# Kernel optimization log

Measured on AMD Instinct MI355X. Metric: run time of the kernel, lower is better.

The kernel has to match this reference:

```python
import jax, jax.numpy as jnp
from jax import lax
import numpy as np

B, POINTS, FEATURES = 8, 32768, 256
F_DIM = FEATURES // 16  # out_dim of query/key 1x1 convs


def setup_inputs() -> dict:
    key = jax.random.key(0)
    ks = jax.random.split(key, 10)
    s = 0.05
    return {
        "x": jax.random.normal(ks[0], (B, POINTS, FEATURES), jnp.float32),
        "Wq": jax.random.normal(ks[1], (F_DIM, FEATURES), jnp.float32) * s,
        "bq": jax.random.normal(ks[2], (F_DIM,), jnp.float32) * s,
        "Wk": jax.random.normal(ks[3], (F_DIM, FEATURES), jnp.float32) * s,
        "bk": jax.random.normal(ks[4], (F_DIM,), jnp.float32) * s,
        "Wv": jax.random.normal(ks[5], (FEATURES, FEATURES), jnp.float32) * s,
        "bv": jax.random.normal(ks[6], (FEATURES,), jnp.float32) * s,
        "Wup": jax.random.normal(ks[7], (1, 1, 3, 3), jnp.float32) * s,  # torch (in,out,kh,kw)
        "bup": jax.random.normal(ks[8], (1,), jnp.float32) * s,
        "gamma": jax.random.normal(ks[9], (), jnp.float32) * 0.1,  # torch inits to 0; nonzero for testing
    }


def _conv_transpose_s16(x, w, b):
    # torch ConvTranspose2d(1,1,kernel=3,stride=16,padding=0,output_padding=13)
    # == dilated conv with lhs_dilation=16, pad (k-1-p, k-1-p+op) = (2,15), flipped kernel
    k = jnp.flip(w, axis=(2, 3)).transpose(1, 0, 2, 3)  # -> OIHW
    y = lax.conv_general_dilated(
        x, k, window_strides=(1, 1), padding=[(2, 15), (2, 15)],
        lhs_dilation=(16, 16), dimension_numbers=("NCHW", "OIHW", "NCHW"))
    return y + b.reshape(1, -1, 1, 1)


def reference(x, Wq, bq, Wk, bk, Wv, bv, Wup, bup, gamma):
    Bm, points, features = x.shape
    f = features // 16
    # torch: x.view(B, features, -1, 1) -- raw memory reinterpretation, not transpose
    x1 = x.reshape(Bm, features, points)
    # 1x1 convs (dilation irrelevant for kernel_size=1) == channel matmuls
    q = jnp.einsum("of,bfp->bop", Wq, x1) + bq[None, :, None]      # (B, f, points)
    k = jnp.einsum("of,bfp->bop", Wk, x1) + bk[None, :, None]      # (B, f, points)
    k = k.reshape(Bm, points, f)                                    # torch .view reinterpretation
    energy = jnp.einsum("bfp,bpg->bfg", q, k)                       # (B, f, f)
    re_scale = _conv_transpose_s16(energy[:, None], Wup, bup)[:, 0]  # (B, features, features)
    attention = jax.nn.softmax(re_scale, axis=1)
    v = jnp.einsum("of,bfp->bop", Wv, x1) + bv[None, :, None]       # (B, features, points)
    v = v.reshape(Bm, points, features)                              # torch .view reinterpretation
    out = jnp.einsum("bpf,bfg->bpg", v, attention)                   # (B, points, features)
    out = gamma * out + x
    return out, attention
```

## Files before the change

kernel.cpp:

```cpp
#include <hip/hip_runtime.h>

#define PTS 32768
#define BP (PTS*256)
#define QKSZ (16*PTS)
#define Q_OFF ((size_t)0)
#define K_OFF ((size_t)4194304)
#define P_OFF ((size_t)8388608)
#define ATT_OFF ((size_t)67108864)
#define WS_V_USH ((size_t)0)
#define WS_ATT_USH ((size_t)67108864)
#define WS_W_USH ((size_t)67633152)
#define WS_NEED ((size_t)135450624)

typedef __attribute__((ext_vector_type(8))) short short8;
typedef __attribute__((ext_vector_type(4))) float f32x4;
typedef __attribute__((ext_vector_type(4))) unsigned short ush4;

__device__ __forceinline__ unsigned short f2bf(float f){
  unsigned u = __float_as_uint(f);
  u += 0x7FFFu + ((u>>16)&1u);
  return (unsigned short)(u>>16);
}

__device__ __forceinline__ void bar_lgkm(){
  asm volatile("s_waitcnt lgkmcnt(0)" ::: "memory");
  __builtin_amdgcn_s_barrier();
}

__global__ void __launch_bounds__(256) k_wprep2(const float* __restrict__ Wv,
    const float* __restrict__ Wq, const float* __restrict__ Wk,
    unsigned short* __restrict__ wimg2){
  int t = blockIdx.x*256 + threadIdx.x;
  if (t >= 9216) return;
  int r = t>>5, qp = t&31;
  const float* src = (r < 256) ? (Wv + (size_t)r*256)
                    : (r < 272) ? (Wq + (size_t)(r-256)*256)
                                : (Wk + (size_t)(r-272)*256);
  int c0 = (qp ^ (r&31))*8;
  short8 h;
  #pragma unroll
  for (int j=0;j<8;j++) h[j] = (short)f2bf(src[c0+j]);
  *(short8*)&wimg2[(size_t)t*8] = h;
}

__global__ void __launch_bounds__(512, 2) k_fused4(const float* __restrict__ x,
    const float* __restrict__ bv, const float* __restrict__ bq, const float* __restrict__ bk,
    const unsigned short* __restrict__ wimg2,
    unsigned short* __restrict__ vws, float* __restrict__ scr){
  __shared__ __align__(16) unsigned short Wl[73728];
  __shared__ __align__(16) float qkT[2048];
  int t = threadIdx.x;
  int w = t>>6, l = t&63;
  int l15 = l&15, l4 = l>>4;

  {
    const short8* src = (const short8*)wimg2;
    short8* dst = (short8*)Wl;
    #pragma unroll
    for (int i=0;i<18;i++) dst[t + 512*i] = src[t + 512*i];
  }
  __syncthreads();

  float* qslice = qkT + w*256;
  float bvv[16];
  #pragma unroll
  for (int mb=0;mb<16;mb++) bvv[mb] = bv[mb*16 + l15];
  float bqv = bq[l15], bkv = bk[l15];

  int gw = blockIdx.x*8 + w;
  for (int it=0; it<4; ++it){
    int tau = gw + 2048*it;
    int b = tau>>10;
    int p0 = (tau&1023)*32;
    const float* xb = x + (size_t)b*BP + p0 + l15;
    f32x4 acc[2][16] = {};
    f32x4 acce[2][2] = {};

    float xv[2][8];
    #pragma unroll
    for (int ps=0; ps<2; ps++)
      #pragma unroll
      for (int j=0;j<8;j++)
        xv[ps][j] = xb[(size_t)(l4*8 + j)*PTS + ps*16];

    for (int kk=0; kk<8; kk++){
      short8 af[2];
      #pragma unroll
      for (int ps=0; ps<2; ps++){
        short8 h;
        #pragma unroll
        for (int j=0;j<8;j++) h[j] = (short)f2bf(xv[ps][j]);
        af[ps] = h;
      }
      if (kk < 7){
        #pragma unroll
        for (int ps=0; ps<2; ps++)
          #pragma unroll
          for (int j=0;j<8;j++)
            xv[ps][j] = xb[(size_t)((kk+1)*32 + l4*8 + j)*PTS + ps*16];
      }
      #pragma unroll
      for (int mb=0; mb<16; mb++){
        int m = mb*16 + l15;
        int phys = (kk*4 + l4) ^ (m&31);
        short8 bf = *(const short8*)&Wl[m*256 + phys*8];
        acc[0][mb] = __builtin_amdgcn_mfma_f32_16x16x32_bf16(af[0], bf, acc[0][mb], 0, 0, 0);
        acc[1][mb] = __builtin_amdgcn_mfma_f32_16x16x32_bf16(af[1], bf, acc[1][mb], 0, 0, 0);
      }
      #pragma unroll
      for (int qs=0; qs<2; qs++){
        int m = 256 + qs*16 + l15;
        int phys = (kk*4 + l4) ^ (m&31);
        short8 bf = *(const short8*)&Wl[m*256 + phys*8];
        acce[0][qs] = __builtin_amdgcn_mfma_f32_16x16x32_bf16(af[0], bf, acce[0][qs], 0, 0, 0);
        acce[1][qs] = __builtin_amdgcn_mfma_f32_16x16x32_bf16(af[1], bf, acce[1][qs], 0, 0, 0);
      }
    }

    unsigned short* vb = vws + (size_t)b*BP;
    #pragma unroll
    for (int ps=0; ps<2; ps++){
      #pragma unroll
      for (int j=0;j<4;j++){
        int p = p0 + ps*16 + l4*4 + j;
        unsigned short* row = vb + (size_t)p*256 + l15;
        #pragma unroll
        for (int mb=0; mb<16; mb++)
          row[mb*16] = f2bf(acc[ps][mb][j] + bvv[mb]);
      }
    }
    #pragma unroll
    for (int ps=0; ps<2; ps++){
      #pragma unroll
      for (int qs=0; qs<2; qs++){
        float bias = qs ? bkv : bqv;
        #pragma unroll
        for (int j=0;j<4;j++){
          int pl = l4*4 + j;
          qslice[pl*16 + (l15 ^ pl)] = acce[ps][qs][j] + bias;
        }
        float* qdst = scr + (qs ? K_OFF : Q_OFF) + (size_t)b*QKSZ;
        #pragma unroll
        for (int r=0;r<4;r++){
          int f = r*4 + l4;
          float v = qslice[l15*16 + (f ^ l15)];
          qdst[(size_t)f*PTS + p0 + ps*16 + l15] = v;
        }
      }
    }
  }
}

__global__ void __launch_bounds__(256) k_energy2(float* __restrict__ scr){
  __shared__ float ql[16][512];
  __shared__ float red[256][17];
  int t = threadIdx.x;
  int ch = blockIdx.x, b = blockIdx.y;
  int pbase = ch*512;
  const float* qb = scr + Q_OFF + (size_t)b*QKSZ;
  #pragma unroll
  for (int i=0;i<8;i++){
    int fid = t + 256*i;
    int f = fid>>7, p4 = fid&127;
    float4 v = *(const float4*)(qb + (size_t)f*PTS + pbase + p4*4);
    *(float4*)&ql[f][p4*4] = v;
  }
  __syncthreads();
  const float* kb = scr + K_OFF + (size_t)b*QKSZ + (size_t)ch*8192;
  float acc[16];
  #pragma unroll
  for (int f=0;f<16;f++) acc[f]=0.f;
  for (int i=0;i<32;i++){
    float kv = kb[i*256 + t];
    int p = i*16 + (t>>4);
    #pragma unroll
    for (int f=0;f<16;f++) acc[f] += kv*ql[f][p];
  }
  #pragma unroll
  for (int f=0;f<16;f++) red[t][f] = acc[f];
  __syncthreads();
  int f = t>>4, g = t&15;
  float s = 0.f;
  #pragma unroll
  for (int k=0;k<16;k++) s += red[g + 16*k][f];
  scr[P_OFF + (size_t)ch*2048 + (size_t)b*256 + t] = s;
}

__global__ void __launch_bounds__(256) k_softmax(float* __restrict__ scr,
    const float* __restrict__ Wup, const float* __restrict__ bup,
    unsigned short* __restrict__ attT){
  __shared__ float el[256];
  int b = blockIdx.x, t = threadIdx.x;
  {
    float s = 0.f;
    for (int ch=0; ch<64; ch++) s += scr[P_OFF + (size_t)ch*2048 + (size_t)b*256 + t];
    el[t] = s;
  }
  __syncthreads();
  int ec = t>>4, kw = t&15;
  float bupv = bup[0];
  bool sp = (kw < 3);
  float w0=0.f,w1=0.f,w2=0.f;
  if (sp){ w0 = Wup[kw]; w1 = Wup[3+kw]; w2 = Wup[6+kw]; }
  float m = bupv;
  float sum;
  if (sp){
    #pragma unroll
    for (int rh=0; rh<16; rh++){
      float e = el[rh*16+ec];
      m = fmaxf(m, fmaxf(fmaxf(w0*e, w1*e), w2*e) + bupv);
    }
    sum = 208.f*__expf(bupv - m);
    for (int rh=0; rh<16; rh++){
      float e = el[rh*16+ec];
      sum += __expf(bupv + w0*e - m) + __expf(bupv + w1*e - m) + __expf(bupv + w2*e - m);
    }
  } else {
    sum = 256.f;
  }
  float inv = 1.f/sum;
  float* attp = scr + ATT_OFF + (size_t)b*65536;
  unsigned short* attTp = attT ? (attT + (size_t)b*65536 + (size_t)t*256) : nullptr;
  for (int r=0; r<256; r++){
    int kh = r&15;
    float v;
    if (sp && kh < 3){
      float e = el[(r>>4)*16 + ec];
      float w = (kh==0)? w0 : ((kh==1)? w1 : w2);
      v = __expf(bupv + w*e - m)*inv;
    } else {
      v = __expf(bupv - m)*inv;
    }
    attp[(size_t)r*256 + t] = v;
    if (attTp) attTp[r] = f2bf(v);
  }
}

__global__ void __launch_bounds__(256, 2) k_out5(const float* __restrict__ x,
    const float* __restrict__ gma,
    const unsigned short* __restrict__ vws,
    const unsigned short* __restrict__ attT,
    float* __restrict__ outb){
  __shared__ __align__(16) unsigned short Vt[32*256];
  __shared__ __align__(16) float Ot[32*260];
  int t = threadIdx.x;
  int b = blockIdx.y;
  int wc = t>>6, l = t&63;
  int l15 = l&15, l4 = l>>4;
  float gm = gma[0];
  const unsigned short* tb = attT + (size_t)b*65536;
  short8 bfv[4][8];
  #pragma unroll
  for (int ni=0;ni<4;ni++){
    int g = wc*64 + ni*16 + l15;
    #pragma unroll
    for (int ks=0;ks<8;ks++)
      bfv[ni][ks] = *(const short8*)(tb + (size_t)g*256 + ks*32 + l4*8);
  }
  short8 vreg[4];
  {
    int p0 = blockIdx.x*32;
    const unsigned short* vsrc = vws + (size_t)b*BP + (size_t)(p0>>7)*PTS + (size_t)(p0&127)*256;
    #pragma unroll
    for (int i=0;i<4;i++) vreg[i] = *(const short8*)(vsrc + (size_t)(i*256+t)*8);
  }
  for (int it=0; it<8; ++it){
    int p0 = (blockIdx.x + 128*it)*32;
    #pragma unroll
    for (int i=0;i<4;i++){
      int idx = i*256 + t;
      int row = idx>>5, chunk = idx&31;
      *(short8*)&Vt[row*256 + ((chunk ^ row)&31)*8] = vreg[i];
    }
    if (it < 7){
      int pn = (blockIdx.x + 128*(it+1))*32;
      const unsigned short* vsrc = vws + (size_t)b*BP + (size_t)(pn>>7)*PTS + (size_t)(pn&127)*256;
      #pragma unroll
      for (int i=0;i<4;i++) vreg[i] = *(const short8*)(vsrc + (size_t)(i*256+t)*8);
    }
    bar_lgkm();
    #pragma unroll
    for (int mi=0;mi<2;mi++){
      int row = mi*16 + l15;
      short8 af[8];
      #pragma unroll
      for (int ks=0;ks<8;ks++){
        int chunk = ks*4 + l4;
        af[ks] = *(const short8*)&Vt[row*256 + ((chunk ^ row)&31)*8];
      }
      #pragma unroll
      for (int ni=0;ni<4;ni++){
        f32x4 acc = {};
        #pragma unroll
        for (int ks=0;ks<8;ks++)
          acc = __builtin_amdgcn_mfma_f32_16x16x32_bf16(af[ks], bfv[ni][ks], acc, 0, 0, 0);
        int gl = wc*64 + ni*16 + l15;
        #pragma unroll
        for (int j=0;j<4;j++)
          Ot[(mi*16 + l4*4 + j)*260 + gl] = acc[j];
      }
    }
    bar_lgkm();
    size_t base = (size_t)b*BP + (size_t)p0*256;
    const float* xb = x + base;
    float* ob = outb + base;
    #pragma unroll
    for (int i=0;i<8;i++){
      int f4 = i*256 + t;
      int row = f4>>6, col = (f4&63)*4;
      float4 a = *(const float4*)&Ot[row*260 + col];
      float4 xv = *(const float4*)(xb + (size_t)f4*4);
      float4 r;
      r.x = gm*a.x + xv.x; r.y = gm*a.y + xv.y;
      r.z = gm*a.z + xv.z; r.w = gm*a.w + xv.w;
      *(float4*)(ob + (size_t)f4*4) = r;
    }
  }
}

__global__ void __launch_bounds__(256) k_qk(const float* __restrict__ x,
    const float* __restrict__ Wq, const float* __restrict__ bq,
    const float* __restrict__ Wk, const float* __restrict__ bk,
    float* __restrict__ scr){
  __shared__ float wlds[256][36];
  int t = threadIdx.x;
  int b = blockIdx.y;
  int p = blockIdx.x*256 + t;
  for (int idx = t; idx < 4096; idx += 256){
    int o = idx>>8, c = idx&255;
    wlds[c][o]    = Wq[idx];
    wlds[c][16+o] = Wk[idx];
  }
  __syncthreads();
  const float* xb = x + (size_t)b*BP;
  float qa[16], ka[16];
  #pragma unroll
  for (int o=0;o<16;o++){ qa[o]=0.f; ka[o]=0.f; }
  for (int c=0;c<256;c++){
    float xv = xb[(size_t)c*PTS + p];
    const float4* wrow = (const float4*)(&wlds[c][0]);
    #pragma unroll
    for (int i=0;i<4;i++){
      float4 wq = wrow[i], wk = wrow[4+i];
      qa[4*i+0] += wq.x*xv; qa[4*i+1] += wq.y*xv; qa[4*i+2] += wq.z*xv; qa[4*i+3] += wq.w*xv;
      ka[4*i+0] += wk.x*xv; ka[4*i+1] += wk.y*xv; ka[4*i+2] += wk.z*xv; ka[4*i+3] += wk.w*xv;
    }
  }
  size_t qb = (size_t)b*QKSZ;
  #pragma unroll
  for (int o=0;o<16;o++){
    scr[Q_OFF + qb + (size_t)o*PTS + p] = qa[o] + bq[o];
    scr[K_OFF + qb + (size_t)o*PTS + p] = ka[o] + bk[o];
  }
}

__global__ void __launch_bounds__(256) k_vgemm(const float* __restrict__ x,
    const float* __restrict__ Wv, const float* __restrict__ bv,
    float* __restrict__ outb){
  __shared__ short At[128][40];
  __shared__ short Bt[128][40];
  int t = threadIdx.x;
  int mt = blockIdx.x, nt = blockIdx.y, b = blockIdx.z;
  const float* xb = x + (size_t)b*BP + (size_t)nt*128;
  const float* Av = Wv + (size_t)mt*128*256;
  int w = t>>6, l = t&63;
  int wr = w>>1, wc = w&1;
  f32x4 acc[4][4] = {};
  int am = t>>1, akq = (t&1)*16;
  int bcl = (t>>4)*2, bn8 = (t&15)*8;

  for (int kk=0; kk<8; kk++){
    int c0 = kk*32;
    {
      const float* s = Av + (size_t)am*256 + c0 + akq;
      float4 v0 = ((const float4*)s)[0];
      float4 v1 = ((const float4*)s)[1];
      float4 v2 = ((const float4*)s)[2];
      float4 v3 = ((const float4*)s)[3];
      short8 h0, h1;
      h0[0]=f2bf(v0.x); h0[1]=f2bf(v0.y); h0[2]=f2bf(v0.z); h0[3]=f2bf(v0.w);
      h0[4]=f2bf(v1.x); h0[5]=f2bf(v1.y); h0[6]=f2bf(v1.z); h0[7]=f2bf(v1.w);
      h1[0]=f2bf(v2.x); h1[1]=f2bf(v2.y); h1[2]=f2bf(v2.z); h1[3]=f2bf(v2.w);
      h1[4]=f2bf(v3.x); h1[5]=f2bf(v3.y); h1[6]=f2bf(v3.z); h1[7]=f2bf(v3.w);
      *(short8*)&At[am][akq]   = h0;
      *(short8*)&At[am][akq+8] = h1;
    }
    {
      const float* s0 = xb + (size_t)(c0+bcl)*PTS + bn8;
      const float* s1 = s0 + PTS;
      float4 a0 = ((const float4*)s0)[0];
      float4 a1 = ((const float4*)s0)[1];
      float4 b0 = ((const float4*)s1)[0];
      float4 b1 = ((const float4*)s1)[1];
      float r0[8] = {a0.x,a0.y,a0.z,a0.w,a1.x,a1.y,a1.z,a1.w};
      float r1[8] = {b0.x,b0.y,b0.z,b0.w,b1.x,b1.y,b1.z,b1.w};
      #pragma unroll
      for (int j=0;j<8;j++){
        unsigned pk = (unsigned)f2bf(r0[j]) | ((unsigned)f2bf(r1[j])<<16);
        *(unsigned*)&Bt[bn8+j][bcl] = pk;
      }
    }
    __syncthreads();
    short8 af[4], bfv[4];
    #pragma unroll
    for (int mi=0;mi<4;mi++) af[mi]  = *(const short8*)&At[64*wr+16*mi+(l&15)][(l>>4)*8];
    #pragma unroll
    for (int ni=0;ni<4;ni++) bfv[ni] = *(const short8*)&Bt[64*wc+16*ni+(l&15)][(l>>4)*8];
    #pragma unroll
    for (int mi=0;mi<4;mi++){
      #pragma unroll
      for (int ni=0;ni<4;ni++)
        acc[mi][ni] = __builtin_amdgcn_mfma_f32_16x16x32_bf16(af[mi], bfv[ni], acc[mi][ni], 0, 0, 0);
    }
    __syncthreads();
  }
  float* ob = outb + (size_t)b*BP;
  #pragma unroll
  for (int mi=0;mi<4;mi++){
    int rbase = mt*128 + 64*wr + 16*mi + ((l>>4)<<2);
    float bvv[4];
    #pragma unroll
    for (int j=0;j<4;j++) bvv[j] = bv[rbase+j];
    #pragma unroll
    for (int ni=0;ni<4;ni++){
      int col = nt*128 + 64*wc + 16*ni + (l&15);
      #pragma unroll
      for (int j=0;j<4;j++)
        ob[(size_t)(rbase+j)*PTS + col] = acc[mi][ni][j] + bvv[j];
    }
  }
}

__global__ void __launch_bounds__(256) k_outgemm(const float* __restrict__ x,
    const float* __restrict__ gma, float* __restrict__ outb){
  __shared__ short Vl[64][264];
  __shared__ short Atl[32][264];
  int t = threadIdx.x;
  int Pq = blockIdx.x, r = blockIdx.y, b = blockIdx.z;
  const float* vsrc = outb + (size_t)b*BP + (size_t)Pq*64*PTS + (size_t)r*256;
  #pragma unroll
  for (int i=0;i<8;i++){
    int row = (t>>5) + 8*i;
    int col = (t&31)*8;
    const float* s = vsrc + (size_t)row*PTS + col;
    float4 v0 = ((const float4*)s)[0];
    float4 v1 = ((const float4*)s)[1];
    short8 h;
    h[0]=f2bf(v0.x); h[1]=f2bf(v0.y); h[2]=f2bf(v0.z); h[3]=f2bf(v0.w);
    h[4]=f2bf(v1.x); h[5]=f2bf(v1.y); h[6]=f2bf(v1.z); h[7]=f2bf(v1.w);
    *(short8*)&Vl[row][col] = h;
  }
  float gm = gma[0];
  const float* attb = outb + ATT_OFF + (size_t)b*65536;
  const float* xb = x + (size_t)b*BP + (size_t)Pq*64*PTS + (size_t)r*256;
  float* ob = outb + (size_t)b*BP + (size_t)Pq*64*PTS + (size_t)r*256;
  int w = t>>6, l = t&63;
  int wr = w>>1, wc = w&1;
  for (int gt=0; gt<8; gt++){
    int g0 = gt*32;
    __syncthreads();
    {
      const float* s = attb + (size_t)t*256 + g0;
      #pragma unroll
      for (int j=0;j<8;j++){
        float4 av = ((const float4*)s)[j];
        Atl[4*j+0][t] = (short)f2bf(av.x);
        Atl[4*j+1][t] = (short)f2bf(av.y);
        Atl[4*j+2][t] = (short)f2bf(av.z);
        Atl[4*j+3][t] = (short)f2bf(av.w);
      }
    }
    __syncthreads();
    f32x4 acc[2] = {};
    #pragma unroll
    for (int ks=0; ks<8; ks++){
      short8 bfrag = *(const short8*)&Atl[16*wc + (l&15)][ks*32 + ((l>>4)<<3)];
      #pragma unroll
      for (int mi=0;mi<2;mi++){
        short8 afrag = *(const short8*)&Vl[32*wr + 16*mi + (l&15)][ks*32 + ((l>>4)<<3)];
        acc[mi] = __builtin_amdgcn_mfma_f32_16x16x32_bf16(afrag, bfrag, acc[mi], 0, 0, 0);
      }
    }
    #pragma unroll
    for (int mi=0;mi<2;mi++){
      int Pl = 32*wr + 16*mi + ((l>>4)<<2);
      int g = g0 + 16*wc + (l&15);
      #pragma unroll
      for (int j=0;j<4;j++){
        size_t a = (size_t)(Pl+j)*PTS + g;
        ob[a] = gm*acc[mi][j] + xb[a];
      }
    }
  }
}

extern "C" void kernel_launch(void* const* d_in, const int* in_sizes, int n_in,
                              void* d_out, int out_size, void* d_ws, size_t ws_size,
                              hipStream_t stream) {
  const float* x   = (const float*)d_in[0];
  const float* Wq  = (const float*)d_in[1];
  const float* bq  = (const float*)d_in[2];
  const float* Wk  = (const float*)d_in[3];
  const float* bk  = (const float*)d_in[4];
  const float* Wv  = (const float*)d_in[5];
  const float* bv  = (const float*)d_in[6];
  const float* Wup = (const float*)d_in[7];
  const float* bup = (const float*)d_in[8];
  const float* gma = (const float*)d_in[9];
  float* out = (float*)d_out;

  bool fast = (d_ws != nullptr) && (ws_size >= WS_NEED);
  unsigned short* vws   = fast ? ((unsigned short*)d_ws) + WS_V_USH   : nullptr;
  unsigned short* attT  = fast ? ((unsigned short*)d_ws) + WS_ATT_USH : nullptr;
  unsigned short* wimg2 = fast ? ((unsigned short*)d_ws) + WS_W_USH   : nullptr;

  if (fast){
    k_wprep2  <<<dim3(36),    256, 0, stream>>>(Wv, Wq, Wk, wimg2);
    k_fused4  <<<dim3(256),   512, 0, stream>>>(x, bv, bq, bk, wimg2, vws, out);
    k_energy2 <<<dim3(64,8),  256, 0, stream>>>(out);
    k_softmax <<<dim3(8),     256, 0, stream>>>(out, Wup, bup, attT);
    k_out5    <<<dim3(128,8), 256, 0, stream>>>(x, gma, vws, attT, out);
  } else {
    k_qk      <<<dim3(128,8),   256, 0, stream>>>(x, Wq, bq, Wk, bk, out);
    k_energy2 <<<dim3(64,8),    256, 0, stream>>>(out);
    k_softmax <<<dim3(8),       256, 0, stream>>>(out, Wup, bup, nullptr);
    k_vgemm   <<<dim3(2,256,8), 256, 0, stream>>>(x, Wv, bv, out);
    k_outgemm <<<dim3(4,128,8), 256, 0, stream>>>(x, gma, out);
  }
}
```

Measured before the change: 286.4 us.

## Split fused projection across two wave groups, shuffle QK transpose, parallelize softmax

The fused V/Q/K projection kernel moves to 1024-thread blocks. Each half of the waves computes half of the V output columns plus either the Q or the K projection, which halves the per-wave accumulator arrays. The LDS-based transpose of the Q/K tile is replaced by ds_bpermute lane shuffles, so the qkT shared buffer goes away. The softmax/attention-write kernel is spread over 8 row chunks per batch (64 blocks instead of 8), with each block recomputing the column statistics. The new launch bound of (1024, 4) could push the compiler to a very tight register budget and cause spills.

New measurement: 712.5 us. +148.8%, slower.

```diff
diff --git a/kernel.cpp b/kernel.cpp
--- a/kernel.cpp
+++ b/kernel.cpp
@@ -43,38 +43,37 @@
   *(short8*)&wimg2[(size_t)t*8] = h;
 }
 
-__global__ void __launch_bounds__(512, 2) k_fused4(const float* __restrict__ x,
+__global__ void __launch_bounds__(1024, 4) k_fused5(const float* __restrict__ x,
     const float* __restrict__ bv, const float* __restrict__ bq, const float* __restrict__ bk,
     const unsigned short* __restrict__ wimg2,
     unsigned short* __restrict__ vws, float* __restrict__ scr){
   __shared__ __align__(16) unsigned short Wl[73728];
-  __shared__ __align__(16) float qkT[2048];
   int t = threadIdx.x;
   int w = t>>6, l = t&63;
+  int g = w>>3, wslot = w&7;
   int l15 = l&15, l4 = l>>4;
 
   {
     const short8* src = (const short8*)wimg2;
     short8* dst = (short8*)Wl;
     #pragma unroll
-    for (int i=0;i<18;i++) dst[t + 512*i] = src[t + 512*i];
+    for (int i=0;i<9;i++) dst[t + 1024*i] = src[t + 1024*i];
   }
   __syncthreads();
 
-  float* qslice = qkT + w*256;
-  float bvv[16];
-  #pragma unroll
-  for (int mb=0;mb<16;mb++) bvv[mb] = bv[mb*16 + l15];
-  float bqv = bq[l15], bkv = bk[l15];
-
-  int gw = blockIdx.x*8 + w;
+  float bvv[8];
+  #pragma unroll
+  for (int mb=0;mb<8;mb++) bvv[mb] = bv[g*128 + mb*16 + l15];
+  float bias = g ? bk[l15] : bq[l15];
+
+  int gw = blockIdx.x*8 + wslot;
   for (int it=0; it<4; ++it){
     int tau = gw + 2048*it;
     int b = tau>>10;
     int p0 = (tau&1023)*32;
     const float* xb = x + (size_t)b*BP + p0 + l15;
-    f32x4 acc[2][16] = {};
-    f32x4 acce[2][2] = {};
+    f32x4 acc[2][8] = {};
+    f32x4 acce[2] = {};
 
     float xv[2][8];
     #pragma unroll
@@ -100,20 +99,19 @@
             xv[ps][j] = xb[(size_t)((kk+1)*32 + l4*8 + j)*PTS + ps*16];
       }
       #pragma unroll
-      for (int mb=0; mb<16; mb++){
-        int m = mb*16 + l15;
+      for (int mb=0; mb<8; mb++){
+        int m = g*128 + mb*16 + l15;
         int phys = (kk*4 + l4) ^ (m&31);
         short8 bf = *(const short8*)&Wl[m*256 + phys*8];
         acc[0][mb] = __builtin_amdgcn_mfma_f32_16x16x32_bf16(af[0], bf, acc[0][mb], 0, 0, 0);
         acc[1][mb] = __builtin_amdgcn_mfma_f32_16x16x32_bf16(af[1], bf, acc[1][mb], 0, 0, 0);
       }
-      #pragma unroll
-      for (int qs=0; qs<2; qs++){
-        int m = 256 + qs*16 + l15;
+      {
+        int m = 256 + g*16 + l15;
         int phys = (kk*4 + l4) ^ (m&31);
         short8 bf = *(const short8*)&Wl[m*256 + phys*8];
-        acce[0][qs] = __builtin_amdgcn_mfma_f32_16x16x32_bf16(af[0], bf, acce[0][qs], 0, 0, 0);
-        acce[1][qs] = __builtin_amdgcn_mfma_f32_16x16x32_bf16(af[1], bf, acce[1][qs], 0, 0, 0);
+        acce[0] = __builtin_amdgcn_mfma_f32_16x16x32_bf16(af[0], bf, acce[0], 0, 0, 0);
+        acce[1] = __builtin_amdgcn_mfma_f32_16x16x32_bf16(af[1], bf, acce[1], 0, 0, 0);
       }
     }
 
@@ -123,29 +121,29 @@
       #pragma unroll
       for (int j=0;j<4;j++){
         int p = p0 + ps*16 + l4*4 + j;
-        unsigned short* row = vb + (size_t)p*256 + l15;
+        unsigned short* row = vb + (size_t)p*256 + g*128 + l15;
         #pragma unroll
-        for (int mb=0; mb<16; mb++)
+        for (int mb=0; mb<8; mb++)
           row[mb*16] = f2bf(acc[ps][mb][j] + bvv[mb]);
       }
     }
+    float* qdst = scr + (g ? K_OFF : Q_OFF) + (size_t)b*QKSZ;
     #pragma unroll
     for (int ps=0; ps<2; ps++){
-      #pragma unroll
-      for (int qs=0; qs<2; qs++){
-        float bias = qs ? bkv : bqv;
-        #pragma unroll
-        for (int j=0;j<4;j++){
-          int pl = l4*4 + j;
-          qslice[pl*16 + (l15 ^ pl)] = acce[ps][qs][j] + bias;
-        }
-        float* qdst = scr + (qs ? K_OFF : Q_OFF) + (size_t)b*QKSZ;
-        #pragma unroll
-        for (int r=0;r<4;r++){
-          int f = r*4 + l4;
-          float v = qslice[l15*16 + (f ^ l15)];
-          qdst[(size_t)f*PTS + p0 + ps*16 + l15] = v;
-        }
+      float vals[4];
+      #pragma unroll
+      for (int j=0;j<4;j++) vals[j] = acce[ps][j] + bias;
+      #pragma unroll
+      for (int r=0;r<4;r++){
+        int f = (l>>4)*4 + r;
+        int lsrc = (((l&15)>>2)<<4) | f;
+        int i0 = __builtin_amdgcn_ds_bpermute(lsrc<<2, __float_as_int(vals[0]));
+        int i1 = __builtin_amdgcn_ds_bpermute(lsrc<<2, __float_as_int(vals[1]));
+        int i2 = __builtin_amdgcn_ds_bpermute(lsrc<<2, __float_as_int(vals[2]));
+        int i3 = __builtin_amdgcn_ds_bpermute(lsrc<<2, __float_as_int(vals[3]));
+        int sel = l&3;
+        int iv = sel==0 ? i0 : sel==1 ? i1 : sel==2 ? i2 : i3;
+        qdst[(size_t)f*PTS + p0 + ps*16 + (l&15)] = __int_as_float(iv);
       }
     }
   }
@@ -186,11 +184,11 @@
   scr[P_OFF + (size_t)ch*2048 + (size_t)b*256 + t] = s;
 }
 
-__global__ void __launch_bounds__(256) k_softmax(float* __restrict__ scr,
+__global__ void __launch_bounds__(256) k_softmax2(float* __restrict__ scr,
     const float* __restrict__ Wup, const float* __restrict__ bup,
     unsigned short* __restrict__ attT){
   __shared__ float el[256];
-  int b = blockIdx.x, t = threadIdx.x;
+  int rc = blockIdx.x, b = blockIdx.y, t = threadIdx.x;
   {
     float s = 0.f;
     for (int ch=0; ch<64; ch++) s += scr[P_OFF + (size_t)ch*2048 + (size_t)b*256 + t];
@@ -221,7 +219,8 @@
   float inv = 1.f/sum;
   float* attp = scr + ATT_OFF + (size_t)b*65536;
   unsigned short* attTp = attT ? (attT + (size_t)b*65536 + (size_t)t*256) : nullptr;
-  for (int r=0; r<256; r++){
+  int r0 = rc*32;
+  for (int r=r0; r<r0+32; r++){
     int kh = r&15;
     float v;
     if (sp && kh < 3){
@@ -260,7 +259,7 @@
   short8 vreg[4];
   {
     int p0 = blockIdx.x*32;
-    const unsigned short* vsrc = vws + (size_t)b*BP + (size_t)(p0>>7)*PTS + (size_t)(p0&127)*256;
+    const unsigned short* vsrc = vws + (size_t)b*BP + (size_t)p0*256;
     #pragma unroll
     for (int i=0;i<4;i++) vreg[i] = *(const short8*)(vsrc + (size_t)(i*256+t)*8);
   }
@@ -274,7 +273,7 @@
     }
     if (it < 7){
       int pn = (blockIdx.x + 128*(it+1))*32;
-      const unsigned short* vsrc = vws + (size_t)b*BP + (size_t)(pn>>7)*PTS + (size_t)(pn&127)*256;
+      const unsigned short* vsrc = vws + (size_t)b*BP + (size_t)pn*256;
       #pragma unroll
       for (int i=0;i<4;i++) vreg[i] = *(const short8*)(vsrc + (size_t)(i*256+t)*8);
     }
@@ -515,15 +514,15 @@
   unsigned short* wimg2 = fast ? ((unsigned short*)d_ws) + WS_W_USH   : nullptr;
 
   if (fast){
-    k_wprep2  <<<dim3(36),    256, 0, stream>>>(Wv, Wq, Wk, wimg2);
-    k_fused4  <<<dim3(256),   512, 0, stream>>>(x, bv, bq, bk, wimg2, vws, out);
-    k_energy2 <<<dim3(64,8),  256, 0, stream>>>(out);
-    k_softmax <<<dim3(8),     256, 0, stream>>>(out, Wup, bup, attT);
-    k_out5    <<<dim3(128,8), 256, 0, stream>>>(x, gma, vws, attT, out);
+    k_wprep2  <<<dim3(36),    256,  0, stream>>>(Wv, Wq, Wk, wimg2);
+    k_fused5  <<<dim3(256),   1024, 0, stream>>>(x, bv, bq, bk, wimg2, vws, out);
+    k_energy2 <<<dim3(64,8),  256,  0, stream>>>(out);
+    k_softmax2<<<dim3(8,8),   256,  0, stream>>>(out, Wup, bup, attT);
+    k_out5    <<<dim3(128,8), 256,  0, stream>>>(x, gma, vws, attT, out);
   } else {
     k_qk      <<<dim3(128,8),   256, 0, stream>>>(x, Wq, bq, Wk, bk, out);
     k_energy2 <<<dim3(64,8),    256, 0, stream>>>(out);
-    k_softmax <<<dim3(8),       256, 0, stream>>>(out, Wup, bup, nullptr);
+    k_softmax2<<<dim3(8,8),     256, 0, stream>>>(out, Wup, bup, nullptr);
     k_vgemm   <<<dim3(2,256,8), 256, 0, stream>>>(x, Wv, bv, out);
     k_outgemm <<<dim3(4,128,8), 256, 0, stream>>>(x, gma, out);
   }
```
